# Kernel tuning notes

Hardware: AMD Instinct MI355X
Metric: run time of the kernel (lower is better)

## Reference

```python
import jax, jax.numpy as jnp
import numpy as np

D_MODEL = 192
NH = 64              # num_harmonics
HQ = 8               # query heads
HKV = 4              # kv heads
DH = D_MODEL // HQ   # d_head = 24
SCALE = 1.0 / float(np.sqrt(DH))
PHASE_TEMP = 1.0


def setup_inputs() -> dict:
    key = jax.random.key(0)
    ks = jax.random.split(key, 4)
    B, S = 2, 2048
    x = jax.random.normal(ks[0], (B, S, D_MODEL), dtype=jnp.float32)
    # Linear weights, bias=False (torch stores as (out, in); y = x @ W.T)
    Wq = jax.random.normal(ks[1], (HQ * DH, D_MODEL), dtype=jnp.float32) * 0.05
    Wkv = jax.random.normal(ks[2], (2 * HKV * DH, D_MODEL), dtype=jnp.float32) * 0.05
    Wo = jax.random.normal(ks[3], (D_MODEL, D_MODEL), dtype=jnp.float32) * 0.05
    alpha = jnp.array(1.0, dtype=jnp.float32)  # blend for standard scores
    beta = jnp.array(0.5, dtype=jnp.float32)   # blend for phase coherence
    return {"x": x, "Wq": Wq, "Wkv": Wkv, "Wo": Wo, "alpha": alpha, "beta": beta}


def reference(x, Wq, Wkv, Wo, alpha, beta):
    B, S, _ = x.shape
    # extract_wave_components: x = [freqs | amps | phases], each (B, S, NH)
    phases = x[..., 2 * NH:]

    # projections
    q = (x @ Wq.T).reshape(B, S, HQ, DH)                 # (B,S,HQ,DH)
    kv = (x @ Wkv.T).reshape(B, S, 2, HKV, DH)
    k, v = kv[:, :, 0], kv[:, :, 1]                      # (B,S,HKV,DH)

    # MQA: repeat_interleave kv heads to HQ heads
    rep = HQ // HKV
    kh = jnp.repeat(k, rep, axis=2)                      # (B,S,HQ,DH)
    vh = jnp.repeat(v, rep, axis=2)

    # standard scaled dot-product scores (B,HQ,Sq,Sk)
    std_scores = jnp.einsum('bqhd,bkhd->bhqk', q, kh) * SCALE

    # cosine phase coherence: mean_h cos(pq - pk)
    #   = (cos(pq)·cos(pk) + sin(pq)·sin(pk)) / NH   -- exact trig identity,
    # avoids materializing the (B,H,Sq,Sk,NH) broadcast-difference tensor.
    # Phases are head-independent (expanded identically across heads in torch),
    # so compute once per batch: (B,Sq,Sk).
    cp, sp = jnp.cos(phases), jnp.sin(phases)            # (B,S,NH)
    coh = (jnp.einsum('bqn,bkn->bqk', cp, cp)
           + jnp.einsum('bqn,bkn->bqk', sp, sp)) / (NH * PHASE_TEMP)

    scores = alpha * std_scores + beta * coh[:, None]    # (B,HQ,Sq,Sk)

    # causal mask
    causal = jnp.tril(jnp.ones((S, S), dtype=bool))
    scores = jnp.where(causal, scores, -1e9)

    attn = jax.nn.softmax(scores, axis=-1)               # (B,HQ,Sq,Sk)
    out = jnp.einsum('bhqk,bkhd->bqhd', attn, vh).reshape(B, S, D_MODEL)
    return out @ Wo.T
```

## Files before the change

### kernel.cpp

```cpp
#include <hip/hip_runtime.h>
#include <math.h>

#define B_N    2
#define S_LEN  2048
#define DMODEL 192
#define LOG2E  1.44269504088896340736f
#define FMAXL2 12.0f

typedef __attribute__((ext_vector_type(8)))  short bf16x8;
typedef __attribute__((ext_vector_type(4)))  float f32x4;
typedef __attribute__((ext_vector_type(16))) float f32x16;

static __device__ __forceinline__ unsigned short f2bf(float f) {
    union { float f; unsigned u; } v; v.f = f;
    unsigned r = v.u + 0x7FFFu + ((v.u >> 16) & 1u);
    return (unsigned short)(r >> 16);
}
static __device__ __forceinline__ unsigned pk2(float a, float b) {
    return (unsigned)f2bf(a) | ((unsigned)f2bf(b) << 16);
}
static __device__ __forceinline__ unsigned cvtpk_bf16(float a, float b) {
    unsigned r;
    asm("v_cvt_pk_bf16_f32 %0, %1, %2" : "=v"(r) : "v"(a), "v"(b));
    return r;
}


__global__ __launch_bounds__(256) void prep_kernel(
    const float* __restrict__ x, const float* __restrict__ Wq,
    const float* __restrict__ Wkv, const float* __restrict__ alpha_p,
    const float* __restrict__ beta_p,
    unsigned short* __restrict__ Qh, unsigned short* __restrict__ Kf,
    unsigned short* __restrict__ Phq, unsigned short* __restrict__ Phf,
    unsigned short* __restrict__ Vf)
{
    __shared__ __align__(16) unsigned short a_lds[64][200];
    __shared__ __align__(16) unsigned short b_lds[64][200];
    const int blk = blockIdx.x, tid = threadIdx.x;

    if (blk < 384) {
        const int wid = tid >> 6, lane = tid & 63, g = lane >> 4, lr = lane & 15;
        const int brow = (blk & 63) * 64;
        const int bcol = (blk >> 6) * 64;

        #pragma unroll
        for (int c = 0; c < 12; ++c) {
            int idx = c * 256 + tid;
            int r = idx / 48, ch = idx % 48;
            float4 v = *(const float4*)&x[(size_t)(brow + r) * 192 + ch * 4];
            uint2 w; w.x = pk2(v.x, v.y); w.y = pk2(v.z, v.w);
            *(uint2*)&a_lds[r][ch * 4] = w;
            int wr = bcol + r;
            const float* wsrc = (wr < 192) ? &Wq[(size_t)wr * 192 + ch * 4]
                                           : &Wkv[(size_t)(wr - 192) * 192 + ch * 4];
            float4 wv = *(const float4*)wsrc;
            uint2 w2; w2.x = pk2(wv.x, wv.y); w2.y = pk2(wv.z, wv.w);
            *(uint2*)&b_lds[r][ch * 4] = w2;
        }
        __syncthreads();

        f32x4 acc[4];
        #pragma unroll
        for (int nc = 0; nc < 4; ++nc) acc[nc] = (f32x4){0.f, 0.f, 0.f, 0.f};
        #pragma unroll
        for (int kc = 0; kc < 6; ++kc) {
            bf16x8 af = *(const bf16x8*)&a_lds[wid * 16 + lr][kc * 32 + g * 8];
            #pragma unroll
            for (int nc = 0; nc < 4; ++nc) {
                bf16x8 bfr = *(const bf16x8*)&b_lds[nc * 16 + lr][kc * 32 + g * 8];
                acc[nc] = __builtin_amdgcn_mfma_f32_16x16x32_bf16(af, bfr, acc[nc], 0, 0, 0);
            }
        }

        const float qs = alpha_p[0] * 0.20412414523193150818f * LOG2E;
        const float scale = (bcol < 192) ? qs : 1.0f;
        __syncthreads();
        unsigned short (*sm)[80] = (unsigned short (*)[80])&a_lds[0][0];
        #pragma unroll
        for (int nc = 0; nc < 4; ++nc)
            #pragma unroll
            for (int rr = 0; rr < 4; ++rr)
                sm[wid * 16 + g * 4 + rr][nc * 16 + lr] = f2bf(acc[nc][rr] * scale);
        __syncthreads();

        #pragma unroll
        for (int pass = 0; pass < 2; ++pass) {
            const int sp = pass * 256 + tid;
            if (bcol < 256) {
                const int cs = sp >> 6, row = sp & 63;
                const int grow = brow + row, b = grow >> 11, s = grow & 2047;
                uint4 v = *(const uint4*)&sm[row][cs * 8];
                const int col = bcol + cs * 8;
                if (bcol < 192) {
                    int h = col / 24, d = col - 24 * h;
                    *(uint4*)(Qh + ((size_t)(b * 8 + h) * S_LEN + s) * 32 + d) = v;
                } else {
                    int cc = col - 192, kvh = cc / 24, d = cc - 24 * kvh;
                    int t = s >> 5, kr = s & 31;
                    *(uint4*)(Kf + (((size_t)(b * 4 + kvh) * 64 + t) * 2 + (d >> 4)) * 512
                              + (kr + 32 * ((d >> 3) & 1)) * 8) = v;
                }
            } else if (bcol == 256) {
                if (sp < 256) {
                    const int cs = sp >> 6, row = sp & 63;
                    const int grow = brow + row, b = grow >> 11, s = grow & 2047;
                    uint4 v = *(const uint4*)&sm[row][cs * 8];
                    const int col = 256 + cs * 8;
                    int cc = col - 192, kvh = cc / 24, d = cc - 24 * kvh;
                    int t = s >> 5, kr = s & 31;
                    *(uint4*)(Kf + (((size_t)(b * 4 + kvh) * 64 + t) * 2 + (d >> 4)) * 512
                              + (kr + 32 * ((d >> 3) & 1)) * 8) = v;
                } else {
                    const int sp2 = sp - 256;
                    const int colL = 32 + (sp2 & 31), r0 = (sp2 >> 5) * 8;
                    const int grow0 = brow + r0, b = grow0 >> 11, s0 = grow0 & 2047;
                    const int col = 256 + colL;
                    int cc = col - 288, kvh = cc / 24, d = cc - 24 * kvh;
                    int t = s0 >> 5, kr0 = s0 & 31;
                    unsigned w0 = (unsigned)sm[r0][colL]     | ((unsigned)sm[r0 + 1][colL] << 16);
                    unsigned w1 = (unsigned)sm[r0 + 2][colL] | ((unsigned)sm[r0 + 3][colL] << 16);
                    unsigned w2 = (unsigned)sm[r0 + 4][colL] | ((unsigned)sm[r0 + 5][colL] << 16);
                    unsigned w3 = (unsigned)sm[r0 + 6][colL] | ((unsigned)sm[r0 + 7][colL] << 16);
                    uint4 v = {w0, w1, w2, w3};
                    *(uint4*)(Vf + (((size_t)(b * 4 + kvh) * 64 + t) * 2 + (kr0 >> 4)) * 512
                              + (d + 32 * ((kr0 >> 3) & 1)) * 8) = v;
                }
            } else {
                const int colL = sp & 63, r0 = (sp >> 6) * 8;
                const int grow0 = brow + r0, b = grow0 >> 11, s0 = grow0 & 2047;
                const int col = 320 + colL;
                int cc = col - 288, kvh = cc / 24, d = cc - 24 * kvh;
                int t = s0 >> 5, kr0 = s0 & 31;
                unsigned w0 = (unsigned)sm[r0][colL]     | ((unsigned)sm[r0 + 1][colL] << 16);
                unsigned w1 = (unsigned)sm[r0 + 2][colL] | ((unsigned)sm[r0 + 3][colL] << 16);
                unsigned w2 = (unsigned)sm[r0 + 4][colL] | ((unsigned)sm[r0 + 5][colL] << 16);
                unsigned w3 = (unsigned)sm[r0 + 6][colL] | ((unsigned)sm[r0 + 7][colL] << 16);
                uint4 v = {w0, w1, w2, w3};
                *(uint4*)(Vf + (((size_t)(b * 4 + kvh) * 64 + t) * 2 + (kr0 >> 4)) * 512
                          + (d + 32 * ((kr0 >> 3) & 1)) * 8) = v;
            }
        }
    } else if (blk < 896) {
        unsigned short (*psm)[128] = (unsigned short (*)[128])&a_lds[0][0];
        const int pblk = blk - 384;
        const int rr = tid >> 5, i = tid & 31;
        const int row = pblk * 8 + rr;
        const int b = row >> 11, s = row & 2047;
        const int t = s >> 5, kr = s & 31;
        const float bf = beta_p[0] * (1.0f / 64.0f) * LOG2E;
        float2 p = *(const float2*)&x[(size_t)row * DMODEL + 128 + 2 * i];
        float s0, c0, s1, c1;
        sincosf(p.x, &s0, &c0);
        sincosf(p.y, &s1, &c1);
        unsigned short* phq = Phq + ((size_t)b * S_LEN + s) * 128;
        *(unsigned*)(phq + 2 * i)      = pk2(c0 * bf, c1 * bf);
        *(unsigned*)(phq + 64 + 2 * i) = pk2(s0 * bf, s1 * bf);
        *(unsigned*)&psm[rr][2 * i]      = pk2(c0, c1);
        *(unsigned*)&psm[rr][64 + 2 * i] = pk2(s0, s1);
        if (i < 12) {
            uint4 z = {0u, 0u, 0u, 0u};
            if (i < 8) {
                *(uint4*)(Qh + ((size_t)(b * 8 + i) * S_LEN + s) * 32 + 24) = z;
            } else {
                int kvh = i - 8;
                *(uint4*)(Kf + (((size_t)(b * 4 + kvh) * 64 + t) * 2 + 1) * 512 + (kr + 32) * 8) = z;
            }
        }
        __syncthreads();
        if (tid < 128) {
            const int krow = tid & 7, d0 = (tid >> 3) * 8;
            const int grow = pblk * 8 + krow, b2 = grow >> 11, s2 = grow & 2047;
            const int t2 = s2 >> 5, kr2 = s2 & 31;
            uint4 v = *(const uint4*)&psm[krow][d0];
            *(uint4*)(Phf + (((size_t)b2 * 64 + t2) * 8 + (d0 >> 4)) * 512
                      + (kr2 + 32 * ((d0 >> 3) & 1)) * 8) = v;
        }
    } else {
        const int j = blk - 896;
        uint4 z = {0u, 0u, 0u, 0u};
        #pragma unroll
        for (int c = 0; c < 8; ++c) {
            int idx = c * 256 + tid;
            int t = idx >> 5, rem = idx & 31;
            int f = rem >> 4, dd = 24 + (rem & 7), hb = (rem >> 3) & 1;
            *(uint4*)(Vf + (((size_t)j * 64 + t) * 2 + f) * 512 + (dd + 32 * hb) * 8) = z;
        }
    }
}

struct KB { bf16x8 kh0, kh1, ph0, ph1, ph2, ph3, ph4, ph5, ph6, ph7, vt0, vt1; };

__global__ __launch_bounds__(64, 2) void attn_kernel(
    const unsigned short* __restrict__ Qh, const unsigned short* __restrict__ Kf,
    const unsigned short* __restrict__ Phq, const unsigned short* __restrict__ Phf,
    const unsigned short* __restrict__ Vf,
    float* __restrict__ pacc, float* __restrict__ pml)
{
    const int lane = threadIdx.x & 63;
    const int hi = lane >> 5, c31 = lane & 31;

    const int bid = blockIdx.x;
    const int grp = bid & 7, b = grp >> 2, kvh = grp & 3;
    const int u = bid >> 3;
    const int quarter = u & 3;
    const int s = 63 - (u >> 2);
    const int r = s + 1;
    const int tb = (quarter * r) >> 2, te = ((quarter + 1) * r) >> 2;
    const int qrow = s * 32 + c31;

    const unsigned short* kf_g = Kf  + (size_t)(b * 4 + kvh) * 65536 + lane * 8;
    const unsigned short* ph_g = Phf + (size_t)b * 262144 + lane * 8;
    const unsigned short* vf_g = Vf  + (size_t)(b * 4 + kvh) * 65536 + lane * 8;

    f32x16 accA = {0,0,0,0,0,0,0,0,0,0,0,0,0,0,0,0};
    f32x16 accB = {0,0,0,0,0,0,0,0,0,0,0,0,0,0,0,0};
    float lA = 0.f, lB = 0.f;

    if (te > tb) {
        bf16x8 qa0, qa1, qb0, qb1, qp[8];
        {
            const unsigned short* q0 = Qh + ((size_t)(b * 8 + 2 * kvh) * S_LEN + qrow) * 32 + hi * 8;
            const unsigned short* q1 = Qh + ((size_t)(b * 8 + 2 * kvh + 1) * S_LEN + qrow) * 32 + hi * 8;
            qa0 = *(const bf16x8*)q0; qa1 = *(const bf16x8*)(q0 + 16);
            qb0 = *(const bf16x8*)q1; qb1 = *(const bf16x8*)(q1 + 16);
            const unsigned short* pq = Phq + ((size_t)b * S_LEN + qrow) * 128 + hi * 8;
            #pragma unroll
            for (int c = 0; c < 8; ++c) qp[c] = *(const bf16x8*)(pq + c * 16);
        }

        auto LOADK = [&](int t) {
            KB kb;
            const unsigned short* kg = kf_g + (size_t)t * 1024;
            const unsigned short* pg = ph_g + (size_t)t * 4096;
            const unsigned short* vg = vf_g + (size_t)t * 1024;
            kb.kh0 = *(const bf16x8*)kg;
            kb.kh1 = *(const bf16x8*)(kg + 512);
            kb.ph0 = *(const bf16x8*)pg;
            kb.ph1 = *(const bf16x8*)(pg + 512);
            kb.ph2 = *(const bf16x8*)(pg + 1024);
            kb.ph3 = *(const bf16x8*)(pg + 1536);
            kb.ph4 = *(const bf16x8*)(pg + 2048);
            kb.ph5 = *(const bf16x8*)(pg + 2560);
            kb.ph6 = *(const bf16x8*)(pg + 3072);
            kb.ph7 = *(const bf16x8*)(pg + 3584);
            kb.vt0 = *(const bf16x8*)vg;
            kb.vt1 = *(const bf16x8*)(vg + 512);
            return kb;
        };

        auto PROCESS = [&](const KB& kb, bf16x8 q0, bf16x8 q1,
                           f32x16& acc, float& l, bool diag) {
            f32x16 sa = {0,0,0,0,0,0,0,0,0,0,0,0,0,0,0,0};
            f32x16 sb = {0,0,0,0,0,0,0,0,0,0,0,0,0,0,0,0};
            sa = __builtin_amdgcn_mfma_f32_32x32x16_bf16(kb.kh0, q0, sa, 0, 0, 0);
            sb = __builtin_amdgcn_mfma_f32_32x32x16_bf16(kb.kh1, q1, sb, 0, 0, 0);
            sa = __builtin_amdgcn_mfma_f32_32x32x16_bf16(kb.ph0, qp[0], sa, 0, 0, 0);
            sb = __builtin_amdgcn_mfma_f32_32x32x16_bf16(kb.ph1, qp[1], sb, 0, 0, 0);
            sa = __builtin_amdgcn_mfma_f32_32x32x16_bf16(kb.ph2, qp[2], sa, 0, 0, 0);
            sb = __builtin_amdgcn_mfma_f32_32x32x16_bf16(kb.ph3, qp[3], sb, 0, 0, 0);
            sa = __builtin_amdgcn_mfma_f32_32x32x16_bf16(kb.ph4, qp[4], sa, 0, 0, 0);
            sb = __builtin_amdgcn_mfma_f32_32x32x16_bf16(kb.ph5, qp[5], sb, 0, 0, 0);
            sa = __builtin_amdgcn_mfma_f32_32x32x16_bf16(kb.ph6, qp[6], sa, 0, 0, 0);
            sb = __builtin_amdgcn_mfma_f32_32x32x16_bf16(kb.ph7, qp[7], sb, 0, 0, 0);
            float p[16];
            #pragma unroll
            for (int i = 0; i < 16; ++i) p[i] = sa[i] + sb[i];
            if (diag) {
                #pragma unroll
                for (int i = 0; i < 16; ++i) {
                    int kr = (i & 3) + 8 * (i >> 2) + 4 * hi;
                    if (kr > c31) p[i] = -1e30f;
                }
            }
            #pragma unroll
            for (int i = 0; i < 16; ++i) p[i] = __builtin_amdgcn_exp2f(p[i] - FMAXL2);
            float u4[4];
            #pragma unroll
            for (int i = 0; i < 4; ++i)
                u4[i] = (p[i] + p[i + 4]) + (p[i + 8] + p[i + 12]);
            l += (u4[0] + u4[1]) + (u4[2] + u4[3]);
            unsigned W[8];
            #pragma unroll
            for (int i = 0; i < 8; ++i) W[i] = cvtpk_bf16(p[2 * i], p[2 * i + 1]);
            union U16 { unsigned d[4]; bf16x8 v; };
#define PVSTEP(e, AV) { \
            unsigned x_  = W[4 * e],     y_  = W[4 * e + 2]; \
            unsigned x2_ = W[4 * e + 1], y2_ = W[4 * e + 3]; \
            asm volatile("v_permlane32_swap_b32 %0, %1" : "+v"(x_),  "+v"(y_)); \
            asm volatile("v_permlane32_swap_b32 %0, %1" : "+v"(x2_), "+v"(y2_)); \
            U16 pf; pf.d[0] = x_; pf.d[1] = x2_; pf.d[2] = y_; pf.d[3] = y2_; \
            acc = __builtin_amdgcn_mfma_f32_32x32x16_bf16(AV, pf.v, acc, 0, 0, 0); }
            PVSTEP(0, kb.vt0)
            PVSTEP(1, kb.vt1)
#undef PVSTEP
        };

        int t = tb;
        KB ka = LOADK(t);
        for (; t + 1 < te; ++t) {
            KB kn = LOADK(t + 1);
            PROCESS(ka, qa0, qa1, accA, lA, false);
            PROCESS(ka, qb0, qb1, accB, lB, false);
            ka = kn;
        }
        const bool dg = (t == r - 1);
        PROCESS(ka, qa0, qa1, accA, lA, dg);
        PROCESS(ka, qb0, qb1, accB, lB, dg);
    }

    {
        float* pa = pacc + (size_t)bid * 2048;
        #pragma unroll
        for (int k = 0; k < 4; ++k) {
            f32x4 v = {accA[4 * k], accA[4 * k + 1], accA[4 * k + 2], accA[4 * k + 3]};
            *(f32x4*)(pa + k * 256 + lane * 4) = v;
        }
        #pragma unroll
        for (int k = 0; k < 4; ++k) {
            f32x4 v = {accB[4 * k], accB[4 * k + 1], accB[4 * k + 2], accB[4 * k + 3]};
            *(f32x4*)(pa + 1024 + k * 256 + lane * 4) = v;
        }
        lA += __shfl_xor(lA, 32, 64);
        lB += __shfl_xor(lB, 32, 64);
        if (hi == 0) {
            pml[(size_t)bid * 64 + c31] = lA;
            pml[(size_t)bid * 64 + 32 + c31] = lB;
        }
    }
}

__global__ __launch_bounds__(64) void combine_kernel(
    const float* __restrict__ pacc, const float* __restrict__ pml,
    unsigned short* __restrict__ Ob)
{
    const int lane = threadIdx.x & 63;
    const int hi = lane >> 5, c31 = lane & 31;
    const int bid = blockIdx.x;
    const int b = bid >> 9, h = (bid >> 6) & 7, s32 = bid & 63;
    const int kvh = h >> 1, hq = h & 1;
    const int grp = b * 4 + kvh;
    const int ubase = ((63 - s32) << 2);

    float L = 0.f;
    float o[16];
    #pragma unroll
    for (int i = 0; i < 16; ++i) o[i] = 0.f;
    #pragma unroll
    for (int i = 0; i < 4; ++i) {
        const int bidp = ((ubase | i) << 3) | grp;
        L += pml[(size_t)bidp * 64 + hq * 32 + c31];
        const float* pa = pacc + (size_t)bidp * 2048 + hq * 1024;
        #pragma unroll
        for (int k = 0; k < 4; ++k) {
            f32x4 v = *(const f32x4*)(pa + k * 256 + lane * 4);
            o[4 * k]     += v[0];
            o[4 * k + 1] += v[1];
            o[4 * k + 2] += v[2];
            o[4 * k + 3] += v[3];
        }
    }
    const float inv = 1.0f / L;

    unsigned short* ob = Ob + ((size_t)b * S_LEN + s32 * 32 + c31) * DMODEL + h * 24 + 4 * hi;
    #pragma unroll
    for (int k = 0; k < 3; ++k) {
        *(unsigned*)(ob + 8 * k)     = pk2(o[4 * k] * inv,     o[4 * k + 1] * inv);
        *(unsigned*)(ob + 8 * k + 2) = pk2(o[4 * k + 2] * inv, o[4 * k + 3] * inv);
    }
}

__global__ __launch_bounds__(256) void proj_gemm_kernel(
    const unsigned short* __restrict__ Ob, const float* __restrict__ Wo,
    float* __restrict__ out)
{
    __shared__ __align__(16) unsigned short a_lds[64][200];
    __shared__ __align__(16) unsigned short b_lds[64][200];
    const int tid = threadIdx.x;
    const int wid = tid >> 6, lane = tid & 63, g = lane >> 4, lr = lane & 15;
    const int brow = blockIdx.x * 64;
    const int bcol = blockIdx.y * 64;

    #pragma unroll
    for (int c = 0; c < 6; ++c) {
        int idx = c * 256 + tid;
        int r = idx / 24, ch = idx % 24;
        *(uint4*)&a_lds[r][ch * 8] = *(const uint4*)&Ob[(size_t)(brow + r) * 192 + ch * 8];
    }
    #pragma unroll
    for (int c = 0; c < 12; ++c) {
        int idx = c * 256 + tid;
        int r = idx / 48, ch = idx % 48;
        float4 wv = *(const float4*)&Wo[(size_t)(bcol + r) * 192 + ch * 4];
        uint2 w2; w2.x = pk2(wv.x, wv.y); w2.y = pk2(wv.z, wv.w);
        *(uint2*)&b_lds[r][ch * 4] = w2;
    }
    __syncthreads();

    f32x4 acc[4];
    #pragma unroll
    for (int nc = 0; nc < 4; ++nc) acc[nc] = (f32x4){0.f, 0.f, 0.f, 0.f};
    #pragma unroll
    for (int kc = 0; kc < 6; ++kc) {
        bf16x8 af = *(const bf16x8*)&a_lds[wid * 16 + lr][kc * 32 + g * 8];
        #pragma unroll
        for (int nc = 0; nc < 4; ++nc) {
            bf16x8 bfr = *(const bf16x8*)&b_lds[nc * 16 + lr][kc * 32 + g * 8];
            acc[nc] = __builtin_amdgcn_mfma_f32_16x16x32_bf16(af, bfr, acc[nc], 0, 0, 0);
        }
    }

    #pragma unroll
    for (int nc = 0; nc < 4; ++nc) {
        int c = bcol + nc * 16 + lr;
        #pragma unroll
        for (int r = 0; r < 4; ++r) {
            int row = brow + wid * 16 + g * 4 + r;
            out[(size_t)row * 192 + c] = acc[nc][r];
        }
    }
}

extern "C" void kernel_launch(void* const* d_in, const int* in_sizes, int n_in,
                              void* d_out, int out_size, void* d_ws, size_t ws_size,
                              hipStream_t stream) {
    const float* x     = (const float*)d_in[0];
    const float* Wq    = (const float*)d_in[1];
    const float* Wkv   = (const float*)d_in[2];
    const float* Wo    = (const float*)d_in[3];
    const float* alpha = (const float*)d_in[4];
    const float* beta  = (const float*)d_in[5];

    char* ws = (char*)d_ws;
    const size_t QH_BYTES  = (size_t)B_N * 8 * S_LEN * 32 * 2;
    const size_t KF_BYTES  = (size_t)B_N * 4 * 65536 * 2;
    const size_t PHQ_BYTES = (size_t)B_N * S_LEN * 128 * 2;
    const size_t PHF_BYTES = (size_t)B_N * 262144 * 2;
    const size_t VF_BYTES  = KF_BYTES;
    const size_t OB_BYTES  = (size_t)B_N * S_LEN * DMODEL * 2;
    const size_t PACC_BYTES = (size_t)2048 * 2048 * 4;

    unsigned short* Qh  = (unsigned short*)ws;
    unsigned short* Kf  = (unsigned short*)(ws + QH_BYTES);
    unsigned short* Phq = (unsigned short*)(ws + QH_BYTES + KF_BYTES);
    unsigned short* Phf = (unsigned short*)(ws + QH_BYTES + KF_BYTES + PHQ_BYTES);
    unsigned short* Vf  = (unsigned short*)(ws + QH_BYTES + KF_BYTES + PHQ_BYTES + PHF_BYTES);
    unsigned short* Ob  = (unsigned short*)(ws + QH_BYTES + KF_BYTES + PHQ_BYTES + PHF_BYTES + VF_BYTES);
    float* pacc = (float*)(ws + QH_BYTES + KF_BYTES + PHQ_BYTES + PHF_BYTES + VF_BYTES + OB_BYTES);
    float* pml  = (float*)(ws + QH_BYTES + KF_BYTES + PHQ_BYTES + PHF_BYTES + VF_BYTES + OB_BYTES + PACC_BYTES);
    float* out = (float*)d_out;

    hipLaunchKernelGGL(prep_kernel, dim3(904), dim3(256), 0, stream,
                       x, Wq, Wkv, alpha, beta, Qh, Kf, Phq, Phf, Vf);
    hipLaunchKernelGGL(attn_kernel, dim3(2048), dim3(64), 0, stream,
                       Qh, Kf, Phq, Phf, Vf, pacc, pml);
    hipLaunchKernelGGL(combine_kernel, dim3(1024), dim3(64), 0, stream,
                       pacc, pml, Ob);
    hipLaunchKernelGGL(proj_gemm_kernel, dim3(64, 3), dim3(256), 0, stream,
                       Ob, Wo, out);
}
```

Before: 41.13 us.

## Split attention blocks per query head instead of sharing K/V across head pair

```diff
diff --git a/kernel.cpp b/kernel.cpp
--- a/kernel.cpp
+++ b/kernel.cpp
@@ -203,7 +203,9 @@
     const int grp = bid & 7, b = grp >> 2, kvh = grp & 3;
     const int u = bid >> 3;
     const int quarter = u & 3;
-    const int s = 63 - (u >> 2);
+    const int hq = (u >> 2) & 1;
+    const int s = 63 - (u >> 3);
+    const int h = 2 * kvh + hq;
     const int r = s + 1;
     const int tb = (quarter * r) >> 2, te = ((quarter + 1) * r) >> 2;
     const int qrow = s * 32 + c31;
@@ -212,17 +214,15 @@
     const unsigned short* ph_g = Phf + (size_t)b * 262144 + lane * 8;
     const unsigned short* vf_g = Vf  + (size_t)(b * 4 + kvh) * 65536 + lane * 8;
 
-    f32x16 accA = {0,0,0,0,0,0,0,0,0,0,0,0,0,0,0,0};
-    f32x16 accB = {0,0,0,0,0,0,0,0,0,0,0,0,0,0,0,0};
-    float lA = 0.f, lB = 0.f;
+    f32x16 acc = {0,0,0,0,0,0,0,0,0,0,0,0,0,0,0,0};
+    float l = 0.f;
 
     if (te > tb) {
-        bf16x8 qa0, qa1, qb0, qb1, qp[8];
+        bf16x8 q0, q1, qp[8];
         {
-            const unsigned short* q0 = Qh + ((size_t)(b * 8 + 2 * kvh) * S_LEN + qrow) * 32 + hi * 8;
-            const unsigned short* q1 = Qh + ((size_t)(b * 8 + 2 * kvh + 1) * S_LEN + qrow) * 32 + hi * 8;
-            qa0 = *(const bf16x8*)q0; qa1 = *(const bf16x8*)(q0 + 16);
-            qb0 = *(const bf16x8*)q1; qb1 = *(const bf16x8*)(q1 + 16);
+            const unsigned short* qh = Qh + ((size_t)(b * 8 + h) * S_LEN + qrow) * 32 + hi * 8;
+            q0 = *(const bf16x8*)qh;
+            q1 = *(const bf16x8*)(qh + 16);
             const unsigned short* pq = Phq + ((size_t)b * S_LEN + qrow) * 128 + hi * 8;
             #pragma unroll
             for (int c = 0; c < 8; ++c) qp[c] = *(const bf16x8*)(pq + c * 16);
@@ -248,8 +248,7 @@
             return kb;
         };
 
-        auto PROCESS = [&](const KB& kb, bf16x8 q0, bf16x8 q1,
-                           f32x16& acc, float& l, bool diag) {
+        auto PROCESS = [&](const KB& kb, bool diag) {
             f32x16 sa = {0,0,0,0,0,0,0,0,0,0,0,0,0,0,0,0};
             f32x16 sb = {0,0,0,0,0,0,0,0,0,0,0,0,0,0,0,0};
             sa = __builtin_amdgcn_mfma_f32_32x32x16_bf16(kb.kh0, q0, sa, 0, 0, 0);
@@ -295,37 +294,21 @@
 #undef PVSTEP
         };
 
-        int t = tb;
-        KB ka = LOADK(t);
-        for (; t + 1 < te; ++t) {
-            KB kn = LOADK(t + 1);
-            PROCESS(ka, qa0, qa1, accA, lA, false);
-            PROCESS(ka, qb0, qb1, accB, lB, false);
-            ka = kn;
-        }
-        const bool dg = (t == r - 1);
-        PROCESS(ka, qa0, qa1, accA, lA, dg);
-        PROCESS(ka, qb0, qb1, accB, lB, dg);
+        for (int t = tb; t < te; ++t) {
+            KB ka = LOADK(t);
+            PROCESS(ka, t == r - 1);
+        }
     }
 
     {
-        float* pa = pacc + (size_t)bid * 2048;
+        float* pa = pacc + (size_t)bid * 1024;
         #pragma unroll
         for (int k = 0; k < 4; ++k) {
-            f32x4 v = {accA[4 * k], accA[4 * k + 1], accA[4 * k + 2], accA[4 * k + 3]};
+            f32x4 v = {acc[4 * k], acc[4 * k + 1], acc[4 * k + 2], acc[4 * k + 3]};
             *(f32x4*)(pa + k * 256 + lane * 4) = v;
         }
-        #pragma unroll
-        for (int k = 0; k < 4; ++k) {
-            f32x4 v = {accB[4 * k], accB[4 * k + 1], accB[4 * k + 2], accB[4 * k + 3]};
-            *(f32x4*)(pa + 1024 + k * 256 + lane * 4) = v;
-        }
-        lA += __shfl_xor(lA, 32, 64);
-        lB += __shfl_xor(lB, 32, 64);
-        if (hi == 0) {
-            pml[(size_t)bid * 64 + c31] = lA;
-            pml[(size_t)bid * 64 + 32 + c31] = lB;
-        }
+        l += __shfl_xor(l, 32, 64);
+        if (hi == 0) pml[(size_t)bid * 32 + c31] = l;
     }
 }
 
@@ -339,7 +322,7 @@
     const int b = bid >> 9, h = (bid >> 6) & 7, s32 = bid & 63;
     const int kvh = h >> 1, hq = h & 1;
     const int grp = b * 4 + kvh;
-    const int ubase = ((63 - s32) << 2);
+    const int ubase = ((63 - s32) << 3) | (hq << 2);
 
     float L = 0.f;
     float o[16];
@@ -347,9 +330,9 @@
     for (int i = 0; i < 16; ++i) o[i] = 0.f;
     #pragma unroll
     for (int i = 0; i < 4; ++i) {
-        const int bidp = ((ubase | i) << 3) | grp;
-        L += pml[(size_t)bidp * 64 + hq * 32 + c31];
-        const float* pa = pacc + (size_t)bidp * 2048 + hq * 1024;
+        const int blk = ((ubase | i) << 3) | grp;
+        L += pml[(size_t)blk * 32 + c31];
+        const float* pa = pacc + (size_t)blk * 1024;
         #pragma unroll
         for (int k = 0; k < 4; ++k) {
             f32x4 v = *(const f32x4*)(pa + k * 256 + lane * 4);
@@ -437,7 +420,7 @@
     const size_t PHF_BYTES = (size_t)B_N * 262144 * 2;
     const size_t VF_BYTES  = KF_BYTES;
     const size_t OB_BYTES  = (size_t)B_N * S_LEN * DMODEL * 2;
-    const size_t PACC_BYTES = (size_t)2048 * 2048 * 4;
+    const size_t PACC_BYTES = (size_t)4096 * 1024 * 4;
 
     unsigned short* Qh  = (unsigned short*)ws;
     unsigned short* Kf  = (unsigned short*)(ws + QH_BYTES);
@@ -451,7 +434,7 @@
 
     hipLaunchKernelGGL(prep_kernel, dim3(904), dim3(256), 0, stream,
                        x, Wq, Wkv, alpha, beta, Qh, Kf, Phq, Phf, Vf);
-    hipLaunchKernelGGL(attn_kernel, dim3(2048), dim3(64), 0, stream,
+    hipLaunchKernelGGL(attn_kernel, dim3(4096), dim3(64), 0, stream,
                        Qh, Kf, Phq, Phf, Vf, pacc, pml);
     hipLaunchKernelGGL(combine_kernel, dim3(1024), dim3(64), 0, stream,
                        pacc, pml, Ob);
```

Result: slower. 48.86 us (+18.8%).
